# Optimization experiments

Hardware: AMD Instinct MI355X
Metric: run time of the kernel (lower is better)

## Reference

```python
import jax, jax.numpy as jnp
import numpy as np

N, C, E, S = 16384, 128, 262144, 10
AVG_NUM_NEIGHBORS = 16.0
INV_SQRT3 = 1.0 / np.sqrt(3.0)


def setup_inputs() -> dict:
    key = jax.random.key(0)
    ks = jax.random.split(key, 15)
    return dict(
        node_specie=jax.random.randint(ks[0], (N,), 0, S),
        node_feats=jax.random.normal(ks[1], (N, C, 4), jnp.float32),   # irreps 0e+1o per channel
        edge_attrs=jax.random.normal(ks[2], (E, 4), jnp.float32),      # Y: 0e+1o
        edge_feats=jax.random.normal(ks[3], (E, 8), jnp.float32),      # radial scalars
        senders=jax.random.randint(ks[4], (E,), 0, N),
        receivers=jax.random.randint(ks[5], (E,), 0, N),
        W_sc0=jax.random.normal(ks[6], (S, C, C), jnp.float32),
        W_sc1=jax.random.normal(ks[7], (S, C, C), jnp.float32),
        W_pre0=jax.random.normal(ks[8], (C, C), jnp.float32),
        W_pre1=jax.random.normal(ks[9], (C, C), jnp.float32),
        W_mlp1=jax.random.normal(ks[10], (8, 64), jnp.float32),
        W_mlp2=jax.random.normal(ks[11], (64, 64), jnp.float32),
        W_mlp3=jax.random.normal(ks[12], (64, 4), jnp.float32),
        W_post0=jax.random.normal(ks[13], (C, 2, C), jnp.float32),
        W_post1=jax.random.normal(ks[14], (C, 2, C), jnp.float32),
    )


def reference(node_specie, node_feats, edge_attrs, edge_feats, senders, receivers,
              W_sc0, W_sc1, W_pre0, W_pre1, W_mlp1, W_mlp2, W_mlp3, W_post0, W_post1):
    inv_c = 1.0 / np.sqrt(C)
    s_in = node_feats[..., 0]      # [N,C] 0e
    v_in = node_feats[..., 1:4]    # [N,C,3] 1o

    # linear_sc: per-species equivariant linear (0e+1o -> hidden 0e+1o)
    sc_s = jnp.einsum('nc,ncd->nd', s_in, W_sc0[node_specie]) * inv_c
    sc_v = jnp.einsum('nci,ncd->ndi', v_in, W_sc1[node_specie]) * inv_c
    sc = jnp.concatenate([sc_s[..., None], sc_v], axis=-1)  # [N,C,4]

    # linear_premp: channel-mixing equivariant linear (same irreps)
    s = (s_in @ W_pre0) * inv_c                              # [N,C]
    v = jnp.einsum('nci,cd->ndi', v_in, W_pre1) * inv_c      # [N,C,3]

    # MessagePassingConvolution (channel axis kept instead of hk.vmap)
    se_s = s[senders]              # [E,C]
    se_v = v[senders]              # [E,C,3]
    a = edge_attrs[:, 1:4]         # drop 0e part of Y -> 1o
    dot = jnp.einsum('eci,ei->ec', se_v, a) * INV_SQRT3      # 1o x 1o -> 0e
    sva = se_s[..., None] * a[:, None, :]                    # 0e x 1o -> 1o

    # radial MLP -> one mixing scalar per irrep (num_irreps = 4), shared across channels
    h = jax.nn.silu((edge_feats @ W_mlp1) * (1.0 / np.sqrt(8.0)))
    h = jax.nn.silu((h @ W_mlp2) * 0.125)
    mix = (h @ W_mlp3) * 0.125                               # [E,4]

    # messages irreps 2x0e+2x1o: [s, dot | v, s*a], each block scaled by its mix scalar
    msg = jnp.concatenate([
        se_s[..., None] * mix[:, None, 0:1],
        dot[..., None] * mix[:, None, 1:2],
        se_v * mix[:, None, 2:3],
        sva * mix[:, None, 3:4],
    ], axis=-1)                                              # [E,C,8]

    agg = jnp.zeros((N, C, 8), msg.dtype).at[receivers].add(msg) / AVG_NUM_NEIGHBORS

    # linear_postmp: (2x0e+2x1o, C channels) -> (0e+1o, C channels)
    inv2c = 1.0 / np.sqrt(2 * C)
    o_s = jnp.einsum('ncm,cmd->nd', agg[..., :2], W_post0) * inv2c
    o_v = jnp.einsum('ncmi,cmd->ndi', agg[..., 2:].reshape(N, C, 2, 3), W_post1) * inv2c
    node_out = jnp.concatenate([o_s[..., None], o_v], axis=-1)  # [N,C,4]
    return node_out, sc
```

## Files before the change

### kernel.cpp

```cpp
#include <hip/hip_runtime.h>
#include <hip/hip_bf16.h>

#define N_NODES 16384
#define C_DIM   128
#define E_EDGES 262144
#define S_SPEC  10
#define CHUNK   256
#define PROWS   16544
#define PTILES  1034

__device__ __constant__ const float INV_C  = 0.08838834764831845f;
__device__ __constant__ const float INV_2C = 0.0625f;
#define F_INV_SQRT3 0.5773502691896258f
#define F_INV_SQRT8 0.35355339059327373f
#define F_INV_AVG   0.0625f

typedef __attribute__((ext_vector_type(8))) short bf16x8;
typedef __attribute__((ext_vector_type(4))) float f32x4;

__device__ __forceinline__ float silu(float x) {
    return x / (1.0f + __expf(-x));
}

__device__ __forceinline__ unsigned short f2bf(float x) {
    __hip_bfloat16 h = __float2bfloat16(x);
    return *reinterpret_cast<unsigned short*>(&h);
}

__device__ __forceinline__ unsigned int pack2bf(float lo, float hi) {
    return (unsigned int)f2bf(lo) | ((unsigned int)f2bf(hi) << 16);
}

__device__ __forceinline__ float bf2f(unsigned short u) {
    return __uint_as_float(((unsigned int)u) << 16);
}

__global__ __launch_bounds__(256) void hist_kernel(
    const int* __restrict__ receivers, int* __restrict__ cnt)
{
    const int e = blockIdx.x * 256 + threadIdx.x;
    atomicAdd(&cnt[receivers[e]], 1);
}

__global__ __launch_bounds__(256) void scan16k_kernel(
    const int* __restrict__ cnt, int* __restrict__ start,
    int* __restrict__ cursor)
{
    __shared__ int sums[256];
    const int t = threadIdx.x;
    int s = 0;
    for (int i = 0; i < 64; ++i) s += cnt[t * 64 + i];
    sums[t] = s;
    __syncthreads();
    if (t == 0) {
        int a = 0;
        for (int i = 0; i < 256; ++i) { int v = sums[i]; sums[i] = a; a += v; }
    }
    __syncthreads();
    int a = sums[t];
    for (int i = 0; i < 64; ++i) {
        int v = cnt[t * 64 + i];
        start[t * 64 + i] = a;
        cursor[t * 64 + i] = a;
        a += v;
    }
    if (t == 255) start[N_NODES] = a;
}

__global__ __launch_bounds__(256) void scatter_kernel(
    const int* __restrict__ receivers, int* __restrict__ cursor,
    int* __restrict__ perm)
{
    const int e = blockIdx.x * 256 + threadIdx.x;
    const int pos = atomicAdd(&cursor[receivers[e]], 1);
    perm[pos] = e;
}

__global__ __launch_bounds__(256) void spec_hist_kernel(
    const int* __restrict__ specie, int* __restrict__ scnt)
{
    __shared__ int h[S_SPEC];
    const int t = threadIdx.x;
    if (t < S_SPEC) h[t] = 0;
    __syncthreads();
    atomicAdd(&h[specie[blockIdx.x * 256 + t]], 1);
    __syncthreads();
    if (t < S_SPEC) atomicAdd(&scnt[t], h[t]);
}

__global__ void spec_scan2_kernel(
    const int* __restrict__ scnt, int* __restrict__ poff,
    int* __restrict__ scur)
{
    if (threadIdx.x == 0) {
        int pa = 0;
        for (int i = 0; i < S_SPEC; ++i) {
            poff[i] = pa;
            scur[i] = 0;
            pa += ((scnt[i] + 15) >> 4) << 4;
        }
    }
}

__global__ __launch_bounds__(256) void spec_place_kernel(
    const int* __restrict__ specie, const int* __restrict__ poff,
    int* __restrict__ scur,
    int* __restrict__ prow_map, int* __restrict__ tile_spec)
{
    __shared__ int h[S_SPEC];
    __shared__ int bbase[S_SPEC];
    const int t = threadIdx.x;
    if (t < S_SPEC) h[t] = 0;
    __syncthreads();
    const int n = blockIdx.x * 256 + t;
    const int s = specie[n];
    const int lrank = atomicAdd(&h[s], 1);
    __syncthreads();
    if (t < S_SPEC && h[t] > 0) bbase[t] = atomicAdd(&scur[t], h[t]);
    __syncthreads();
    const int p = poff[s] + bbase[s] + lrank;
    prow_map[p] = n;
    tile_spec[p >> 4] = s;
}

__global__ __launch_bounds__(256) void node_in_convert_kernel(
    const int* __restrict__ prow_map, const float* __restrict__ node_feats,
    ushort* __restrict__ As, ushort* __restrict__ Av0,
    ushort* __restrict__ Av1, ushort* __restrict__ Av2)
{
    const int idx = blockIdx.x * 256 + threadIdx.x;
    const int p = idx >> 7, c = idx & 127;
    const int nid = prow_map[p];
    float4 f = {0.0f, 0.0f, 0.0f, 0.0f};
    if (nid >= 0) f = ((const float4*)node_feats)[nid * C_DIM + c];
    As [idx] = f2bf(f.x);
    Av0[idx] = f2bf(f.y);
    Av1[idx] = f2bf(f.z);
    Av2[idx] = f2bf(f.w);
}

__global__ __launch_bounds__(256) void wsc_convert_kernel(
    const float* __restrict__ Wsc0, const float* __restrict__ Wsc1,
    ushort* __restrict__ W0t, ushort* __restrict__ W1t_)
{
    const int idx = blockIdx.x * 256 + threadIdx.x;
    const int s = idx >> 14, d = (idx >> 7) & 127, k = idx & 127;
    W0t [idx] = f2bf(Wsc0[s * 16384 + k * 128 + d] * INV_C);
    W1t_[idx] = f2bf(Wsc1[s * 16384 + k * 128 + d] * INV_C);
}

__global__ __launch_bounds__(256) void wpre_convert_kernel(
    const float* __restrict__ Wpre0, const float* __restrict__ Wpre1,
    ushort* __restrict__ P0t, ushort* __restrict__ P1t)
{
    const int idx = blockIdx.x * 256 + threadIdx.x;
    const int d = idx >> 7, k = idx & 127;
    P0t[idx] = f2bf(Wpre0[k * 128 + d] * INV_C);
    P1t[idx] = f2bf(Wpre1[k * 128 + d] * INV_C);
}

__global__ __launch_bounds__(256) void wpost_convert_kernel(
    const float* __restrict__ W0, const float* __restrict__ W1,
    ushort* __restrict__ Bt0, ushort* __restrict__ Bt1)
{
    const int idx = blockIdx.x * 256 + threadIdx.x;
    const int k = idx >> 7, d = idx & 127;
    Bt0[d * 256 + k] = f2bf(W0[idx] * INV_2C);
    Bt1[d * 256 + k] = f2bf(W1[idx] * INV_2C);
}

__global__ __launch_bounds__(256) void wmlp_convert_kernel(
    const float* __restrict__ W1, const float* __restrict__ W2,
    const float* __restrict__ W3,
    ushort* __restrict__ W1t, ushort* __restrict__ W2t,
    ushort* __restrict__ W3t)
{
    const int idx = blockIdx.x * 256 + threadIdx.x;
    if (idx < 2048) {
        const int h = idx >> 5, k = idx & 31;
        W1t[idx] = (k < 8) ? f2bf(W1[k * 64 + h] * F_INV_SQRT8) : (ushort)0;
    }
    {
        const int c = idx >> 6, k = idx & 63;
        W2t[idx] = f2bf(W2[k * 64 + c] * 0.125f);
    }
    if (idx < 1024) {
        const int m = idx >> 6, k = idx & 63;
        W3t[idx] = (m < 4) ? f2bf(W3[k * 4 + m] * 0.125f) : (ushort)0;
    }
}

__global__ __launch_bounds__(512) void node_gemm_kernel(
    const int* __restrict__ prow_map,
    const int* __restrict__ tile_spec,
    const ushort* __restrict__ As,
    const ushort* __restrict__ Av0,
    const ushort* __restrict__ Av1,
    const ushort* __restrict__ Av2,
    const ushort* __restrict__ Wsc0t,
    const ushort* __restrict__ Wsc1t,
    const ushort* __restrict__ Wpre0t,
    const ushort* __restrict__ Wpre1t,
    float* __restrict__ out_sc,
    ushort4* __restrict__ sv_bf)
{
    const int l  = threadIdx.x & 63;
    const int w  = threadIdx.x >> 6;
    const int d0 = w * 16;
    const int lr = l & 15;
    const int lg = l >> 4;

    bf16x8 bp0[4], bp1[4];
#pragma unroll
    for (int ks = 0; ks < 4; ++ks) {
        bp0[ks] = *reinterpret_cast<const bf16x8*>(
            Wpre0t + (d0 + lr) * 128 + ks * 32 + lg * 8);
        bp1[ks] = *reinterpret_cast<const bf16x8*>(
            Wpre1t + (d0 + lr) * 128 + ks * 32 + lg * 8);
    }

    const int tile = blockIdx.x;
    const int sp   = tile_spec[tile];
    const int r0   = tile * 16;

    const ushort* as  = As  + (size_t)(r0 + lr) * 128 + lg * 8;
    const ushort* av0 = Av0 + (size_t)(r0 + lr) * 128 + lg * 8;
    const ushort* av1 = Av1 + (size_t)(r0 + lr) * 128 + lg * 8;
    const ushort* av2 = Av2 + (size_t)(r0 + lr) * 128 + lg * 8;
    const ushort* ws0 = Wsc0t + (size_t)sp * 16384 + (d0 + lr) * 128 + lg * 8;
    const ushort* ws1 = Wsc1t + (size_t)sp * 16384 + (d0 + lr) * 128 + lg * 8;

    const f32x4 zero = {0.0f, 0.0f, 0.0f, 0.0f};
    f32x4 aS0 = zero, aS1 = zero, aS2 = zero, aS3 = zero;
    f32x4 aP0 = zero, aP1 = zero, aP2 = zero, aP3 = zero;

#pragma unroll
    for (int ks = 0; ks < 4; ++ks) {
        const bf16x8 a_s  = *reinterpret_cast<const bf16x8*>(as  + ks * 32);
        const bf16x8 a_v0 = *reinterpret_cast<const bf16x8*>(av0 + ks * 32);
        const bf16x8 a_v1 = *reinterpret_cast<const bf16x8*>(av1 + ks * 32);
        const bf16x8 a_v2 = *reinterpret_cast<const bf16x8*>(av2 + ks * 32);
        const bf16x8 bs0  = *reinterpret_cast<const bf16x8*>(ws0 + ks * 32);
        const bf16x8 bs1  = *reinterpret_cast<const bf16x8*>(ws1 + ks * 32);
        aS0 = __builtin_amdgcn_mfma_f32_16x16x32_bf16(a_s,  bs0, aS0, 0, 0, 0);
        aS1 = __builtin_amdgcn_mfma_f32_16x16x32_bf16(a_v0, bs1, aS1, 0, 0, 0);
        aS2 = __builtin_amdgcn_mfma_f32_16x16x32_bf16(a_v1, bs1, aS2, 0, 0, 0);
        aS3 = __builtin_amdgcn_mfma_f32_16x16x32_bf16(a_v2, bs1, aS3, 0, 0, 0);
        aP0 = __builtin_amdgcn_mfma_f32_16x16x32_bf16(a_s,  bp0[ks], aP0, 0, 0, 0);
        aP1 = __builtin_amdgcn_mfma_f32_16x16x32_bf16(a_v0, bp1[ks], aP1, 0, 0, 0);
        aP2 = __builtin_amdgcn_mfma_f32_16x16x32_bf16(a_v1, bp1[ks], aP2, 0, 0, 0);
        aP3 = __builtin_amdgcn_mfma_f32_16x16x32_bf16(a_v2, bp1[ks], aP3, 0, 0, 0);
    }

#pragma unroll
    for (int r = 0; r < 4; ++r) {
        const int row = r0 + lg * 4 + r;
        const int nid = prow_map[row];
        if (nid >= 0) {
            float4 o = {aS0[r], aS1[r], aS2[r], aS3[r]};
            ((float4*)out_sc)[(size_t)nid * C_DIM + (d0 + lr)] = o;
            ushort4 pv = {f2bf(aP0[r]), f2bf(aP1[r]), f2bf(aP2[r]), f2bf(aP3[r])};
            sv_bf[(size_t)nid * C_DIM + (d0 + lr)] = pv;
        }
    }
}

__global__ __launch_bounds__(256) void edge_mlp_mfma_kernel(
    const float* __restrict__ edge_feats,
    const float* __restrict__ edge_attrs,
    const ushort* __restrict__ W1t,
    const ushort* __restrict__ W2t,
    const ushort* __restrict__ W3t,
    float* __restrict__ coef)
{
    __shared__ ushort h_lds[4][16][72];

    const int w  = threadIdx.x >> 6;
    const int l  = threadIdx.x & 63;
    const int lr = l & 15;
    const int lg = l >> 4;

    bf16x8 a1[4];
#pragma unroll
    for (int mt = 0; mt < 4; ++mt)
        a1[mt] = *reinterpret_cast<const bf16x8*>(
            W1t + (mt * 16 + lr) * 32 + lg * 8);
    bf16x8 a2[4][2];
#pragma unroll
    for (int mt = 0; mt < 4; ++mt)
#pragma unroll
        for (int ks = 0; ks < 2; ++ks)
            a2[mt][ks] = *reinterpret_cast<const bf16x8*>(
                W2t + (mt * 16 + lr) * 64 + ks * 32 + lg * 8);
    bf16x8 a3[2];
#pragma unroll
    for (int ks = 0; ks < 2; ++ks)
        a3[ks] = *reinterpret_cast<const bf16x8*>(
            W3t + lr * 64 + ks * 32 + lg * 8);

    const int tile = blockIdx.x * 4 + w;
    const int e0   = tile * 16;
    const f32x4 zero = {0.0f, 0.0f, 0.0f, 0.0f};

    bf16x8 b1 = {0, 0, 0, 0, 0, 0, 0, 0};
    if (lg == 0) {
        const float4 q0 = *(const float4*)(edge_feats + (size_t)(e0 + lr) * 8);
        const float4 q1 = *(const float4*)(edge_feats + (size_t)(e0 + lr) * 8 + 4);
        b1[0] = (short)f2bf(q0.x); b1[1] = (short)f2bf(q0.y);
        b1[2] = (short)f2bf(q0.z); b1[3] = (short)f2bf(q0.w);
        b1[4] = (short)f2bf(q1.x); b1[5] = (short)f2bf(q1.y);
        b1[6] = (short)f2bf(q1.z); b1[7] = (short)f2bf(q1.w);
    }

    f32x4 d1[4];
#pragma unroll
    for (int mt = 0; mt < 4; ++mt)
        d1[mt] = __builtin_amdgcn_mfma_f32_16x16x32_bf16(a1[mt], b1, zero, 0, 0, 0);

#pragma unroll
    for (int mt = 0; mt < 4; ++mt) {
        uint2 p;
        p.x = pack2bf(silu(d1[mt][0]), silu(d1[mt][1]));
        p.y = pack2bf(silu(d1[mt][2]), silu(d1[mt][3]));
        *reinterpret_cast<uint2*>(&h_lds[w][lr][mt * 16 + lg * 4]) = p;
    }
    __syncthreads();

    bf16x8 b2[2];
#pragma unroll
    for (int ks = 0; ks < 2; ++ks)
        b2[ks] = *reinterpret_cast<const bf16x8*>(
            &h_lds[w][lr][ks * 32 + lg * 8]);

    f32x4 d2[4];
#pragma unroll
    for (int mt = 0; mt < 4; ++mt) {
        d2[mt] = __builtin_amdgcn_mfma_f32_16x16x32_bf16(a2[mt][0], b2[0], zero, 0, 0, 0);
        d2[mt] = __builtin_amdgcn_mfma_f32_16x16x32_bf16(a2[mt][1], b2[1], d2[mt], 0, 0, 0);
    }

#pragma unroll
    for (int mt = 0; mt < 4; ++mt) {
        uint2 p;
        p.x = pack2bf(silu(d2[mt][0]), silu(d2[mt][1]));
        p.y = pack2bf(silu(d2[mt][2]), silu(d2[mt][3]));
        *reinterpret_cast<uint2*>(&h_lds[w][lr][mt * 16 + lg * 4]) = p;
    }
    __syncthreads();

    bf16x8 b3[2];
#pragma unroll
    for (int ks = 0; ks < 2; ++ks)
        b3[ks] = *reinterpret_cast<const bf16x8*>(
            &h_lds[w][lr][ks * 32 + lg * 8]);

    f32x4 d3;
    d3 = __builtin_amdgcn_mfma_f32_16x16x32_bf16(a3[0], b3[0], zero, 0, 0, 0);
    d3 = __builtin_amdgcn_mfma_f32_16x16x32_bf16(a3[1], b3[1], d3, 0, 0, 0);

    if (lg == 0) {
        const int e = e0 + lr;
        const float4 a = *(const float4*)(edge_attrs + (size_t)e * 4);
        const float mx0 = d3[0], mx1 = d3[1], mx2 = d3[2], mx3 = d3[3];
        float4 c0 = {mx0, mx1 * a.y * F_INV_SQRT3,
                     mx1 * a.z * F_INV_SQRT3, mx1 * a.w * F_INV_SQRT3};
        float4 c1 = {mx2, mx3 * a.y, mx3 * a.z, mx3 * a.w};
        ((float4*)coef)[e * 2 + 0] = c0;
        ((float4*)coef)[e * 2 + 1] = c1;
    }
}

__global__ __launch_bounds__(256) void agg_kernel(
    const int* __restrict__ start,
    const int* __restrict__ perm,
    const int* __restrict__ senders,
    const float* __restrict__ coef,
    const ushort4* __restrict__ sv_bf,
    unsigned int* __restrict__ A_s,
    unsigned int* __restrict__ A_v)
{
    __shared__ int   se_lds[CHUNK];
    __shared__ float sc_lds[CHUNK][8];

    const int n0   = blockIdx.x * 8;
    const int t    = threadIdx.x;
    const int c    = t & 127;
    const int half = t >> 7;

    int nbeg[4], nend[4];
#pragma unroll
    for (int k = 0; k < 4; ++k) {
        nbeg[k] = start[n0 + half * 4 + k];
        nend[k] = start[n0 + half * 4 + k + 1];
    }

    const int blk_beg = start[n0];
    const int blk_end = start[n0 + 8];
    const float4* coef4 = (const float4*)coef;

    float acc[4][8] = {};

    for (int cb = blk_beg; cb < blk_end; cb += CHUNK) {
        const int cn = min(CHUNK, blk_end - cb);
        __syncthreads();
        for (int j = t; j < cn; j += 256) {
            const int e = perm[cb + j];
            se_lds[j] = senders[e];
            ((float4*)sc_lds[j])[0] = coef4[e * 2 + 0];
            ((float4*)sc_lds[j])[1] = coef4[e * 2 + 1];
        }
        __syncthreads();

#pragma unroll
        for (int k = 0; k < 4; ++k) {
            const int lo = max(nbeg[k], cb);
            const int hi = min(nend[k], cb + cn);
            int idx = lo;
            for (; idx + 2 <= hi; idx += 2) {
                const int j0 = idx - cb, j1 = j0 + 1;
                const int snd0 = se_lds[j0];
                const int snd1 = se_lds[j1];
                const ushort4 u0 = sv_bf[snd0 * C_DIM + c];
                const ushort4 u1 = sv_bf[snd1 * C_DIM + c];
                const float* kf0 = sc_lds[j0];
                const float* kf1 = sc_lds[j1];
                const float x0 = bf2f(u0.x), y0 = bf2f(u0.y),
                            z0 = bf2f(u0.z), w0 = bf2f(u0.w);
                const float x1 = bf2f(u1.x), y1 = bf2f(u1.y),
                            z1 = bf2f(u1.z), w1 = bf2f(u1.w);
                acc[k][0] += x0 * kf0[0];
                acc[k][1] += y0 * kf0[1] + z0 * kf0[2] + w0 * kf0[3];
                acc[k][2] += y0 * kf0[4];
                acc[k][3] += z0 * kf0[4];
                acc[k][4] += w0 * kf0[4];
                acc[k][5] += x0 * kf0[5];
                acc[k][6] += x0 * kf0[6];
                acc[k][7] += x0 * kf0[7];
                acc[k][0] += x1 * kf1[0];
                acc[k][1] += y1 * kf1[1] + z1 * kf1[2] + w1 * kf1[3];
                acc[k][2] += y1 * kf1[4];
                acc[k][3] += z1 * kf1[4];
                acc[k][4] += w1 * kf1[4];
                acc[k][5] += x1 * kf1[5];
                acc[k][6] += x1 * kf1[6];
                acc[k][7] += x1 * kf1[7];
            }
            if (idx < hi) {
                const int j = idx - cb;
                const int snd = se_lds[j];
                const ushort4 u = sv_bf[snd * C_DIM + c];
                const float* kf = sc_lds[j];
                const float x = bf2f(u.x), y = bf2f(u.y),
                            z = bf2f(u.z), w = bf2f(u.w);
                acc[k][0] += x * kf[0];
                acc[k][1] += y * kf[1] + z * kf[2] + w * kf[3];
                acc[k][2] += y * kf[4];
                acc[k][3] += z * kf[4];
                acc[k][4] += w * kf[4];
                acc[k][5] += x * kf[5];
                acc[k][6] += x * kf[6];
                acc[k][7] += x * kf[7];
            }
        }
    }

#pragma unroll
    for (int k = 0; k < 4; ++k) {
        const int n = n0 + half * 4 + k;
        A_s[n * 128 + c] = pack2bf(acc[k][0] * F_INV_AVG, acc[k][1] * F_INV_AVG);
        A_v[(n * 3 + 0) * 128 + c] =
            pack2bf(acc[k][2] * F_INV_AVG, acc[k][5] * F_INV_AVG);
        A_v[(n * 3 + 1) * 128 + c] =
            pack2bf(acc[k][3] * F_INV_AVG, acc[k][6] * F_INV_AVG);
        A_v[(n * 3 + 2) * 128 + c] =
            pack2bf(acc[k][4] * F_INV_AVG, acc[k][7] * F_INV_AVG);
    }
}

__global__ __launch_bounds__(512) void post_gemm_kernel(
    const ushort* __restrict__ A,
    const ushort* __restrict__ Bt,
    float* __restrict__ out,
    int ntiles, int rows_per_node, int comp_base)
{
    const int l  = threadIdx.x & 63;
    const int w  = threadIdx.x >> 6;
    const int d0 = w * 16;
    const int lr = l & 15;
    const int lg = l >> 4;

    bf16x8 bfrag[8];
#pragma unroll
    for (int ks = 0; ks < 8; ++ks) {
        bfrag[ks] = *reinterpret_cast<const bf16x8*>(
            Bt + (size_t)(d0 + lr) * 256 + ks * 32 + lg * 8);
    }

    for (int tile = blockIdx.x; tile < ntiles; tile += gridDim.x) {
        const int r0 = tile * 16;
        f32x4 acc = {0.0f, 0.0f, 0.0f, 0.0f};
        const ushort* ap = A + (size_t)(r0 + lr) * 256 + lg * 8;
#pragma unroll
        for (int ks = 0; ks < 8; ++ks) {
            bf16x8 a = *reinterpret_cast<const bf16x8*>(ap + ks * 32);
            acc = __builtin_amdgcn_mfma_f32_16x16x32_bf16(a, bfrag[ks], acc,
                                                          0, 0, 0);
        }
#pragma unroll
        for (int r = 0; r < 4; ++r) {
            const int row = r0 + lg * 4 + r;
            int n, comp;
            if (rows_per_node == 1) { n = row; comp = 0; }
            else { n = row / 3; comp = comp_base + (row - n * 3); }
            out[(size_t)n * 512 + (d0 + lr) * 4 + comp] = acc[r];
        }
    }
}

extern "C" void kernel_launch(void* const* d_in, const int* in_sizes, int n_in,
                              void* d_out, int out_size, void* d_ws, size_t ws_size,
                              hipStream_t stream)
{
    const int*   specie     = (const int*)d_in[0];
    const float* node_feats = (const float*)d_in[1];
    const float* edge_attrs = (const float*)d_in[2];
    const float* edge_feats = (const float*)d_in[3];
    const int*   senders    = (const int*)d_in[4];
    const int*   receivers  = (const int*)d_in[5];
    const float* Wsc0  = (const float*)d_in[6];
    const float* Wsc1  = (const float*)d_in[7];
    const float* Wpre0 = (const float*)d_in[8];
    const float* Wpre1 = (const float*)d_in[9];
    const float* Wm1   = (const float*)d_in[10];
    const float* Wm2   = (const float*)d_in[11];
    const float* Wm3   = (const float*)d_in[12];
    const float* Wp0   = (const float*)d_in[13];
    const float* Wp1   = (const float*)d_in[14];

    float* out_node = (float*)d_out;
    float* out_sc   = out_node + (size_t)N_NODES * C_DIM * 4;

    char* ws = (char*)d_ws;
    ushort4*      sv_bf = (ushort4*)ws;
    unsigned int* A_s   = (unsigned int*)(ws + (size_t)16 * 1024 * 1024);
    unsigned int* A_v   = A_s + (size_t)N_NODES * 128;
    float*        coef  = (float*)(A_v + (size_t)3 * N_NODES * 128);
    ushort*       Asin  = (ushort*)(coef + (size_t)E_EDGES * 8);
    ushort*       Av0in = Asin  + (size_t)PROWS * 128;
    ushort*       Av1in = Av0in + (size_t)PROWS * 128;
    ushort*       Av2in = Av1in + (size_t)PROWS * 128;
    ushort*       Bt0   = Av2in + (size_t)PROWS * 128;
    ushort*       Bt1   = Bt0 + 256 * 128;
    ushort*       Wsc0t = Bt1 + 256 * 128;
    ushort*       Wsc1t = Wsc0t + S_SPEC * 128 * 128;
    ushort*       Wpre0t = Wsc1t + S_SPEC * 128 * 128;
    ushort*       Wpre1t = Wpre0t + 128 * 128;
    ushort*       W1t   = Wpre1t + 128 * 128;
    ushort*       W2t   = W1t + 64 * 32;
    ushort*       W3t   = W2t + 64 * 64;
    int* counts    = (int*)(W3t + 16 * 64);
    int* start     = counts + N_NODES;
    int* cursor    = start + (N_NODES + 1);
    int* perm      = cursor + N_NODES;
    int* scnt      = perm + E_EDGES;
    int* poff      = scnt + S_SPEC;
    int* scur      = poff + S_SPEC;
    int* prow_map  = scur + S_SPEC;
    int* tile_spec = prow_map + PROWS;

    hipMemsetAsync(counts, 0, N_NODES * sizeof(int), stream);
    hipMemsetAsync(scnt, 0, S_SPEC * sizeof(int), stream);
    hipMemsetAsync(prow_map, 0xFF, PROWS * sizeof(int), stream);
    hipMemsetAsync(tile_spec, 0, PTILES * sizeof(int), stream);

    hist_kernel<<<E_EDGES / 256, 256, 0, stream>>>(receivers, counts);
    scan16k_kernel<<<1, 256, 0, stream>>>(counts, start, cursor);
    scatter_kernel<<<E_EDGES / 256, 256, 0, stream>>>(receivers, cursor, perm);

    spec_hist_kernel<<<N_NODES / 256, 256, 0, stream>>>(specie, scnt);
    spec_scan2_kernel<<<1, 64, 0, stream>>>(scnt, poff, scur);
    spec_place_kernel<<<N_NODES / 256, 256, 0, stream>>>(
        specie, poff, scur, prow_map, tile_spec);

    node_in_convert_kernel<<<PROWS * 128 / 256, 256, 0, stream>>>(
        prow_map, node_feats, Asin, Av0in, Av1in, Av2in);
    wsc_convert_kernel<<<S_SPEC * 128 * 128 / 256, 256, 0, stream>>>(
        Wsc0, Wsc1, Wsc0t, Wsc1t);
    wpre_convert_kernel<<<64, 256, 0, stream>>>(Wpre0, Wpre1, Wpre0t, Wpre1t);
    wpost_convert_kernel<<<128, 256, 0, stream>>>(Wp0, Wp1, Bt0, Bt1);
    wmlp_convert_kernel<<<16, 256, 0, stream>>>(Wm1, Wm2, Wm3, W1t, W2t, W3t);

    node_gemm_kernel<<<PTILES, 512, 0, stream>>>(
        prow_map, tile_spec, Asin, Av0in, Av1in, Av2in,
        Wsc0t, Wsc1t, Wpre0t, Wpre1t, out_sc, sv_bf);

    edge_mlp_mfma_kernel<<<E_EDGES / 64, 256, 0, stream>>>(
        edge_feats, edge_attrs, W1t, W2t, W3t, coef);

    agg_kernel<<<N_NODES / 8, 256, 0, stream>>>(
        start, perm, senders, coef, sv_bf, A_s, A_v);

    post_gemm_kernel<<<512, 512, 0, stream>>>(
        (const ushort*)A_s, Bt0, out_node, N_NODES / 16, 1, 0);
    post_gemm_kernel<<<1024, 512, 0, stream>>>(
        (const ushort*)A_v, Bt1, out_node, 3 * N_NODES / 16, 3, 1);
}
```

Measured before the change: 264.3 us.

## Merge setup kernels, restructure aggregation to wave-per-node, fuse post GEMMs

New measurement: 236.2 us. -10.6%, faster.

```diff
diff --git a/kernel.cpp b/kernel.cpp
--- a/kernel.cpp
+++ b/kernel.cpp
@@ -5,7 +5,6 @@
 #define C_DIM   128
 #define E_EDGES 262144
 #define S_SPEC  10
-#define CHUNK   256
 #define PROWS   16544
 #define PTILES  1034
 
@@ -31,23 +30,57 @@
     return (unsigned int)f2bf(lo) | ((unsigned int)f2bf(hi) << 16);
 }
 
-__device__ __forceinline__ float bf2f(unsigned short u) {
-    return __uint_as_float(((unsigned int)u) << 16);
+__device__ __forceinline__ float bf2f(unsigned int u16) {
+    return __uint_as_float(u16 << 16);
+}
+
+__global__ __launch_bounds__(256) void init_kernel(
+    int* __restrict__ counts, int* __restrict__ scnt,
+    int* __restrict__ prow_map, int* __restrict__ tile_spec)
+{
+    const int idx = blockIdx.x * 256 + threadIdx.x;
+    if (idx < N_NODES) counts[idx] = 0;
+    if (idx < S_SPEC)  scnt[idx] = 0;
+    if (idx < PROWS)   prow_map[idx] = -1;
+    if (idx < PTILES)  tile_spec[idx] = 0;
 }
 
 __global__ __launch_bounds__(256) void hist_kernel(
-    const int* __restrict__ receivers, int* __restrict__ cnt)
-{
-    const int e = blockIdx.x * 256 + threadIdx.x;
+    const int* __restrict__ receivers, int* __restrict__ cnt,
+    const int* __restrict__ specie, int* __restrict__ scnt)
+{
+    __shared__ int h[S_SPEC];
+    const int t = threadIdx.x;
+    const bool doSpec = blockIdx.x < (N_NODES / 256);
+    if (doSpec) {
+        if (t < S_SPEC) h[t] = 0;
+        __syncthreads();
+        atomicAdd(&h[specie[blockIdx.x * 256 + t]], 1);
+    }
+    const int e = blockIdx.x * 256 + t;
     atomicAdd(&cnt[receivers[e]], 1);
-}
-
-__global__ __launch_bounds__(256) void scan16k_kernel(
+    if (doSpec) {
+        __syncthreads();
+        if (t < S_SPEC) atomicAdd(&scnt[t], h[t]);
+    }
+}
+
+__global__ __launch_bounds__(256) void scan_kernel(
     const int* __restrict__ cnt, int* __restrict__ start,
-    int* __restrict__ cursor)
+    int* __restrict__ cursor,
+    const int* __restrict__ scnt, int* __restrict__ poff,
+    int* __restrict__ scur)
 {
     __shared__ int sums[256];
     const int t = threadIdx.x;
+    if (t == 0) {
+        int pa = 0;
+        for (int i = 0; i < S_SPEC; ++i) {
+            poff[i] = pa;
+            scur[i] = 0;
+            pa += ((scnt[i] + 15) >> 4) << 4;
+        }
+    }
     int s = 0;
     for (int i = 0; i < 64; ++i) s += cnt[t * 64 + i];
     sums[t] = s;
@@ -67,126 +100,89 @@
     if (t == 255) start[N_NODES] = a;
 }
 
-__global__ __launch_bounds__(256) void scatter_kernel(
+__global__ __launch_bounds__(256) void scatter_place_kernel(
     const int* __restrict__ receivers, int* __restrict__ cursor,
-    int* __restrict__ perm)
-{
-    const int e = blockIdx.x * 256 + threadIdx.x;
-    const int pos = atomicAdd(&cursor[receivers[e]], 1);
-    perm[pos] = e;
-}
-
-__global__ __launch_bounds__(256) void spec_hist_kernel(
-    const int* __restrict__ specie, int* __restrict__ scnt)
-{
-    __shared__ int h[S_SPEC];
-    const int t = threadIdx.x;
-    if (t < S_SPEC) h[t] = 0;
-    __syncthreads();
-    atomicAdd(&h[specie[blockIdx.x * 256 + t]], 1);
-    __syncthreads();
-    if (t < S_SPEC) atomicAdd(&scnt[t], h[t]);
-}
-
-__global__ void spec_scan2_kernel(
-    const int* __restrict__ scnt, int* __restrict__ poff,
-    int* __restrict__ scur)
-{
-    if (threadIdx.x == 0) {
-        int pa = 0;
-        for (int i = 0; i < S_SPEC; ++i) {
-            poff[i] = pa;
-            scur[i] = 0;
-            pa += ((scnt[i] + 15) >> 4) << 4;
-        }
-    }
-}
-
-__global__ __launch_bounds__(256) void spec_place_kernel(
+    int* __restrict__ perm,
     const int* __restrict__ specie, const int* __restrict__ poff,
     int* __restrict__ scur,
     int* __restrict__ prow_map, int* __restrict__ tile_spec)
 {
-    __shared__ int h[S_SPEC];
-    __shared__ int bbase[S_SPEC];
     const int t = threadIdx.x;
-    if (t < S_SPEC) h[t] = 0;
-    __syncthreads();
-    const int n = blockIdx.x * 256 + t;
-    const int s = specie[n];
-    const int lrank = atomicAdd(&h[s], 1);
-    __syncthreads();
-    if (t < S_SPEC && h[t] > 0) bbase[t] = atomicAdd(&scur[t], h[t]);
-    __syncthreads();
-    const int p = poff[s] + bbase[s] + lrank;
-    prow_map[p] = n;
-    tile_spec[p >> 4] = s;
-}
-
-__global__ __launch_bounds__(256) void node_in_convert_kernel(
+    const int e = blockIdx.x * 256 + t;
+    const int pos = atomicAdd(&cursor[receivers[e]], 1);
+    perm[pos] = e;
+
+    if (blockIdx.x < (N_NODES / 256)) {
+        __shared__ int h[S_SPEC];
+        __shared__ int bbase[S_SPEC];
+        if (t < S_SPEC) h[t] = 0;
+        __syncthreads();
+        const int n = blockIdx.x * 256 + t;
+        const int s = specie[n];
+        const int lrank = atomicAdd(&h[s], 1);
+        __syncthreads();
+        if (t < S_SPEC && h[t] > 0) bbase[t] = atomicAdd(&scur[t], h[t]);
+        __syncthreads();
+        const int p = poff[s] + bbase[s] + lrank;
+        prow_map[p] = n;
+        tile_spec[p >> 4] = s;
+    }
+}
+
+__global__ __launch_bounds__(256) void prep_kernel(
     const int* __restrict__ prow_map, const float* __restrict__ node_feats,
     ushort* __restrict__ As, ushort* __restrict__ Av0,
-    ushort* __restrict__ Av1, ushort* __restrict__ Av2)
-{
-    const int idx = blockIdx.x * 256 + threadIdx.x;
-    const int p = idx >> 7, c = idx & 127;
-    const int nid = prow_map[p];
-    float4 f = {0.0f, 0.0f, 0.0f, 0.0f};
-    if (nid >= 0) f = ((const float4*)node_feats)[nid * C_DIM + c];
-    As [idx] = f2bf(f.x);
-    Av0[idx] = f2bf(f.y);
-    Av1[idx] = f2bf(f.z);
-    Av2[idx] = f2bf(f.w);
-}
-
-__global__ __launch_bounds__(256) void wsc_convert_kernel(
+    ushort* __restrict__ Av1, ushort* __restrict__ Av2,
     const float* __restrict__ Wsc0, const float* __restrict__ Wsc1,
-    ushort* __restrict__ W0t, ushort* __restrict__ W1t_)
-{
-    const int idx = blockIdx.x * 256 + threadIdx.x;
-    const int s = idx >> 14, d = (idx >> 7) & 127, k = idx & 127;
-    W0t [idx] = f2bf(Wsc0[s * 16384 + k * 128 + d] * INV_C);
-    W1t_[idx] = f2bf(Wsc1[s * 16384 + k * 128 + d] * INV_C);
-}
-
-__global__ __launch_bounds__(256) void wpre_convert_kernel(
+    ushort* __restrict__ Wsc0t, ushort* __restrict__ Wsc1t,
     const float* __restrict__ Wpre0, const float* __restrict__ Wpre1,
-    ushort* __restrict__ P0t, ushort* __restrict__ P1t)
-{
-    const int idx = blockIdx.x * 256 + threadIdx.x;
-    const int d = idx >> 7, k = idx & 127;
-    P0t[idx] = f2bf(Wpre0[k * 128 + d] * INV_C);
-    P1t[idx] = f2bf(Wpre1[k * 128 + d] * INV_C);
-}
-
-__global__ __launch_bounds__(256) void wpost_convert_kernel(
-    const float* __restrict__ W0, const float* __restrict__ W1,
-    ushort* __restrict__ Bt0, ushort* __restrict__ Bt1)
-{
-    const int idx = blockIdx.x * 256 + threadIdx.x;
-    const int k = idx >> 7, d = idx & 127;
-    Bt0[d * 256 + k] = f2bf(W0[idx] * INV_2C);
-    Bt1[d * 256 + k] = f2bf(W1[idx] * INV_2C);
-}
-
-__global__ __launch_bounds__(256) void wmlp_convert_kernel(
-    const float* __restrict__ W1, const float* __restrict__ W2,
-    const float* __restrict__ W3,
+    ushort* __restrict__ Wpre0t, ushort* __restrict__ Wpre1t,
+    const float* __restrict__ Wp0, const float* __restrict__ Wp1,
+    ushort* __restrict__ Bt0, ushort* __restrict__ Bt1,
+    const float* __restrict__ Wm1, const float* __restrict__ Wm2,
+    const float* __restrict__ Wm3,
     ushort* __restrict__ W1t, ushort* __restrict__ W2t,
     ushort* __restrict__ W3t)
 {
     const int idx = blockIdx.x * 256 + threadIdx.x;
-    if (idx < 2048) {
-        const int h = idx >> 5, k = idx & 31;
-        W1t[idx] = (k < 8) ? f2bf(W1[k * 64 + h] * F_INV_SQRT8) : (ushort)0;
-    }
     {
-        const int c = idx >> 6, k = idx & 63;
-        W2t[idx] = f2bf(W2[k * 64 + c] * 0.125f);
-    }
-    if (idx < 1024) {
-        const int m = idx >> 6, k = idx & 63;
-        W3t[idx] = (m < 4) ? f2bf(W3[k * 4 + m] * 0.125f) : (ushort)0;
+        const int p = idx >> 7, c = idx & 127;
+        const int nid = prow_map[p];
+        float4 f = {0.0f, 0.0f, 0.0f, 0.0f};
+        if (nid >= 0) f = ((const float4*)node_feats)[nid * C_DIM + c];
+        As [idx] = f2bf(f.x);
+        Av0[idx] = f2bf(f.y);
+        Av1[idx] = f2bf(f.z);
+        Av2[idx] = f2bf(f.w);
+    }
+    if (idx < S_SPEC * 128 * 128) {
+        const int s = idx >> 14, d = (idx >> 7) & 127, k = idx & 127;
+        Wsc0t[idx] = f2bf(Wsc0[s * 16384 + k * 128 + d] * INV_C);
+        Wsc1t[idx] = f2bf(Wsc1[s * 16384 + k * 128 + d] * INV_C);
+    }
+    if (idx < 16384) {
+        const int d = idx >> 7, k = idx & 127;
+        Wpre0t[idx] = f2bf(Wpre0[k * 128 + d] * INV_C);
+        Wpre1t[idx] = f2bf(Wpre1[k * 128 + d] * INV_C);
+    }
+    if (idx < 32768) {
+        const int k = idx >> 7, d = idx & 127;
+        Bt0[d * 256 + k] = f2bf(Wp0[idx] * INV_2C);
+        Bt1[d * 256 + k] = f2bf(Wp1[idx] * INV_2C);
+    }
+    if (idx < 4096) {
+        if (idx < 2048) {
+            const int hh = idx >> 5, k = idx & 31;
+            W1t[idx] = (k < 8) ? f2bf(Wm1[k * 64 + hh] * F_INV_SQRT8) : (ushort)0;
+        }
+        {
+            const int c = idx >> 6, k = idx & 63;
+            W2t[idx] = f2bf(Wm2[k * 64 + c] * 0.125f);
+        }
+        if (idx < 1024) {
+            const int m = idx >> 6, k = idx & 63;
+            W3t[idx] = (m < 4) ? f2bf(Wm3[k * 4 + m] * 0.125f) : (ushort)0;
+        }
     }
 }
 
@@ -375,113 +371,88 @@
     const int* __restrict__ perm,
     const int* __restrict__ senders,
     const float* __restrict__ coef,
-    const ushort4* __restrict__ sv_bf,
+    const uint4* __restrict__ sv16,
     unsigned int* __restrict__ A_s,
     unsigned int* __restrict__ A_v)
 {
-    __shared__ int   se_lds[CHUNK];
-    __shared__ float sc_lds[CHUNK][8];
-
-    const int n0   = blockIdx.x * 8;
-    const int t    = threadIdx.x;
-    const int c    = t & 127;
-    const int half = t >> 7;
-
-    int nbeg[4], nend[4];
-#pragma unroll
-    for (int k = 0; k < 4; ++k) {
-        nbeg[k] = start[n0 + half * 4 + k];
-        nend[k] = start[n0 + half * 4 + k + 1];
-    }
-
-    const int blk_beg = start[n0];
-    const int blk_end = start[n0 + 8];
+    const int n    = blockIdx.x * 4 + (threadIdx.x >> 6);
+    const int lane = threadIdx.x & 63;
+
+    const int beg = start[n];
+    const int end = start[n + 1];
     const float4* coef4 = (const float4*)coef;
 
-    float acc[4][8] = {};
-
-    for (int cb = blk_beg; cb < blk_end; cb += CHUNK) {
-        const int cn = min(CHUNK, blk_end - cb);
-        __syncthreads();
-        for (int j = t; j < cn; j += 256) {
-            const int e = perm[cb + j];
-            se_lds[j] = senders[e];
-            ((float4*)sc_lds[j])[0] = coef4[e * 2 + 0];
-            ((float4*)sc_lds[j])[1] = coef4[e * 2 + 1];
-        }
-        __syncthreads();
-
-#pragma unroll
-        for (int k = 0; k < 4; ++k) {
-            const int lo = max(nbeg[k], cb);
-            const int hi = min(nend[k], cb + cn);
-            int idx = lo;
-            for (; idx + 2 <= hi; idx += 2) {
-                const int j0 = idx - cb, j1 = j0 + 1;
-                const int snd0 = se_lds[j0];
-                const int snd1 = se_lds[j1];
-                const ushort4 u0 = sv_bf[snd0 * C_DIM + c];
-                const ushort4 u1 = sv_bf[snd1 * C_DIM + c];
-                const float* kf0 = sc_lds[j0];
-                const float* kf1 = sc_lds[j1];
-                const float x0 = bf2f(u0.x), y0 = bf2f(u0.y),
-                            z0 = bf2f(u0.z), w0 = bf2f(u0.w);
-                const float x1 = bf2f(u1.x), y1 = bf2f(u1.y),
-                            z1 = bf2f(u1.z), w1 = bf2f(u1.w);
-                acc[k][0] += x0 * kf0[0];
-                acc[k][1] += y0 * kf0[1] + z0 * kf0[2] + w0 * kf0[3];
-                acc[k][2] += y0 * kf0[4];
-                acc[k][3] += z0 * kf0[4];
-                acc[k][4] += w0 * kf0[4];
-                acc[k][5] += x0 * kf0[5];
-                acc[k][6] += x0 * kf0[6];
-                acc[k][7] += x0 * kf0[7];
-                acc[k][0] += x1 * kf1[0];
-                acc[k][1] += y1 * kf1[1] + z1 * kf1[2] + w1 * kf1[3];
-                acc[k][2] += y1 * kf1[4];
-                acc[k][3] += z1 * kf1[4];
-                acc[k][4] += w1 * kf1[4];
-                acc[k][5] += x1 * kf1[5];
-                acc[k][6] += x1 * kf1[6];
-                acc[k][7] += x1 * kf1[7];
-            }
-            if (idx < hi) {
-                const int j = idx - cb;
-                const int snd = se_lds[j];
-                const ushort4 u = sv_bf[snd * C_DIM + c];
-                const float* kf = sc_lds[j];
-                const float x = bf2f(u.x), y = bf2f(u.y),
-                            z = bf2f(u.z), w = bf2f(u.w);
-                acc[k][0] += x * kf[0];
-                acc[k][1] += y * kf[1] + z * kf[2] + w * kf[3];
-                acc[k][2] += y * kf[4];
-                acc[k][3] += z * kf[4];
-                acc[k][4] += w * kf[4];
-                acc[k][5] += x * kf[5];
-                acc[k][6] += x * kf[6];
-                acc[k][7] += x * kf[7];
-            }
-        }
-    }
-
-#pragma unroll
-    for (int k = 0; k < 4; ++k) {
-        const int n = n0 + half * 4 + k;
-        A_s[n * 128 + c] = pack2bf(acc[k][0] * F_INV_AVG, acc[k][1] * F_INV_AVG);
-        A_v[(n * 3 + 0) * 128 + c] =
-            pack2bf(acc[k][2] * F_INV_AVG, acc[k][5] * F_INV_AVG);
-        A_v[(n * 3 + 1) * 128 + c] =
-            pack2bf(acc[k][3] * F_INV_AVG, acc[k][6] * F_INV_AVG);
-        A_v[(n * 3 + 2) * 128 + c] =
-            pack2bf(acc[k][4] * F_INV_AVG, acc[k][7] * F_INV_AVG);
-    }
+    float acc0[8] = {};
+    float acc1[8] = {};
+
+    int e_nx = 0, s_nx = 0;
+    if (beg < end) {
+        e_nx = __builtin_amdgcn_readfirstlane(perm[beg]);
+        s_nx = __builtin_amdgcn_readfirstlane(senders[e_nx]);
+    }
+
+    for (int idx = beg; idx < end; ++idx) {
+        const int e   = e_nx;
+        const int snd = s_nx;
+        if (idx + 1 < end) {
+            e_nx = __builtin_amdgcn_readfirstlane(perm[idx + 1]);
+            s_nx = __builtin_amdgcn_readfirstlane(senders[e_nx]);
+        }
+        const float4 k0 = coef4[(size_t)e * 2 + 0];
+        const float4 k1 = coef4[(size_t)e * 2 + 1];
+        const uint4  q  = sv16[(size_t)snd * 64 + lane];
+
+        const float x0 = bf2f(q.x & 0xffff), y0 = bf2f(q.x >> 16);
+        const float z0 = bf2f(q.y & 0xffff), w0 = bf2f(q.y >> 16);
+        const float x1 = bf2f(q.z & 0xffff), y1 = bf2f(q.z >> 16);
+        const float z1 = bf2f(q.w & 0xffff), w1 = bf2f(q.w >> 16);
+
+        acc0[0] += x0 * k0.x;
+        acc0[1] += y0 * k0.y + z0 * k0.z + w0 * k0.w;
+        acc0[2] += y0 * k1.x;
+        acc0[3] += z0 * k1.x;
+        acc0[4] += w0 * k1.x;
+        acc0[5] += x0 * k1.y;
+        acc0[6] += x0 * k1.z;
+        acc0[7] += x0 * k1.w;
+
+        acc1[0] += x1 * k0.x;
+        acc1[1] += y1 * k0.y + z1 * k0.z + w1 * k0.w;
+        acc1[2] += y1 * k1.x;
+        acc1[3] += z1 * k1.x;
+        acc1[4] += w1 * k1.x;
+        acc1[5] += x1 * k1.y;
+        acc1[6] += x1 * k1.z;
+        acc1[7] += x1 * k1.w;
+    }
+
+    uint2 vs;
+    vs.x = pack2bf(acc0[0] * F_INV_AVG, acc0[1] * F_INV_AVG);
+    vs.y = pack2bf(acc1[0] * F_INV_AVG, acc1[1] * F_INV_AVG);
+    ((uint2*)A_s)[(size_t)n * 64 + lane] = vs;
+
+    uint2 v0;
+    v0.x = pack2bf(acc0[2] * F_INV_AVG, acc0[5] * F_INV_AVG);
+    v0.y = pack2bf(acc1[2] * F_INV_AVG, acc1[5] * F_INV_AVG);
+    ((uint2*)A_v)[((size_t)n * 3 + 0) * 64 + lane] = v0;
+
+    uint2 v1;
+    v1.x = pack2bf(acc0[3] * F_INV_AVG, acc0[6] * F_INV_AVG);
+    v1.y = pack2bf(acc1[3] * F_INV_AVG, acc1[6] * F_INV_AVG);
+    ((uint2*)A_v)[((size_t)n * 3 + 1) * 64 + lane] = v1;
+
+    uint2 v2;
+    v2.x = pack2bf(acc0[4] * F_INV_AVG, acc0[7] * F_INV_AVG);
+    v2.y = pack2bf(acc1[4] * F_INV_AVG, acc1[7] * F_INV_AVG);
+    ((uint2*)A_v)[((size_t)n * 3 + 2) * 64 + lane] = v2;
 }
 
 __global__ __launch_bounds__(512) void post_gemm_kernel(
-    const ushort* __restrict__ A,
-    const ushort* __restrict__ Bt,
-    float* __restrict__ out,
-    int ntiles, int rows_per_node, int comp_base)
+    const ushort* __restrict__ A_s,
+    const ushort* __restrict__ A_v,
+    const ushort* __restrict__ Bt0,
+    const ushort* __restrict__ Bt1,
+    float* __restrict__ out)
 {
     const int l  = threadIdx.x & 63;
     const int w  = threadIdx.x >> 6;
@@ -489,6 +460,13 @@
     const int lr = l & 15;
     const int lg = l >> 4;
 
+    const bool isS = blockIdx.x < 512;
+    const ushort* A  = isS ? A_s : A_v;
+    const ushort* Bt = isS ? Bt0 : Bt1;
+    const int ntiles  = isS ? (N_NODES / 16) : (3 * N_NODES / 16);
+    const int b0      = isS ? blockIdx.x : blockIdx.x - 512;
+    const int gstride = isS ? 512 : 1024;
+
     bf16x8 bfrag[8];
 #pragma unroll
     for (int ks = 0; ks < 8; ++ks) {
@@ -496,7 +474,7 @@
             Bt + (size_t)(d0 + lr) * 256 + ks * 32 + lg * 8);
     }
 
-    for (int tile = blockIdx.x; tile < ntiles; tile += gridDim.x) {
+    for (int tile = b0; tile < ntiles; tile += gstride) {
         const int r0 = tile * 16;
         f32x4 acc = {0.0f, 0.0f, 0.0f, 0.0f};
         const ushort* ap = A + (size_t)(r0 + lr) * 256 + lg * 8;
@@ -510,8 +488,8 @@
         for (int r = 0; r < 4; ++r) {
             const int row = r0 + lg * 4 + r;
             int n, comp;
-            if (rows_per_node == 1) { n = row; comp = 0; }
-            else { n = row / 3; comp = comp_base + (row - n * 3); }
+            if (isS) { n = row; comp = 0; }
+            else { n = row / 3; comp = 1 + (row - n * 3); }
             out[(size_t)n * 512 + (d0 + lr) * 4 + comp] = acc[r];
         }
     }
@@ -568,27 +546,21 @@
     int* prow_map  = scur + S_SPEC;
     int* tile_spec = prow_map + PROWS;
 
-    hipMemsetAsync(counts, 0, N_NODES * sizeof(int), stream);
-    hipMemsetAsync(scnt, 0, S_SPEC * sizeof(int), stream);
-    hipMemsetAsync(prow_map, 0xFF, PROWS * sizeof(int), stream);
-    hipMemsetAsync(tile_spec, 0, PTILES * sizeof(int), stream);
-
-    hist_kernel<<<E_EDGES / 256, 256, 0, stream>>>(receivers, counts);
-    scan16k_kernel<<<1, 256, 0, stream>>>(counts, start, cursor);
-    scatter_kernel<<<E_EDGES / 256, 256, 0, stream>>>(receivers, cursor, perm);
-
-    spec_hist_kernel<<<N_NODES / 256, 256, 0, stream>>>(specie, scnt);
-    spec_scan2_kernel<<<1, 64, 0, stream>>>(scnt, poff, scur);
-    spec_place_kernel<<<N_NODES / 256, 256, 0, stream>>>(
-        specie, poff, scur, prow_map, tile_spec);
-
-    node_in_convert_kernel<<<PROWS * 128 / 256, 256, 0, stream>>>(
-        prow_map, node_feats, Asin, Av0in, Av1in, Av2in);
-    wsc_convert_kernel<<<S_SPEC * 128 * 128 / 256, 256, 0, stream>>>(
-        Wsc0, Wsc1, Wsc0t, Wsc1t);
-    wpre_convert_kernel<<<64, 256, 0, stream>>>(Wpre0, Wpre1, Wpre0t, Wpre1t);
-    wpost_convert_kernel<<<128, 256, 0, stream>>>(Wp0, Wp1, Bt0, Bt1);
-    wmlp_convert_kernel<<<16, 256, 0, stream>>>(Wm1, Wm2, Wm3, W1t, W2t, W3t);
+    init_kernel<<<(PROWS + 255) / 256, 256, 0, stream>>>(
+        counts, scnt, prow_map, tile_spec);
+
+    hist_kernel<<<E_EDGES / 256, 256, 0, stream>>>(
+        receivers, counts, specie, scnt);
+
+    scan_kernel<<<1, 256, 0, stream>>>(counts, start, cursor, scnt, poff, scur);
+
+    scatter_place_kernel<<<E_EDGES / 256, 256, 0, stream>>>(
+        receivers, cursor, perm, specie, poff, scur, prow_map, tile_spec);
+
+    prep_kernel<<<PROWS * 128 / 256, 256, 0, stream>>>(
+        prow_map, node_feats, Asin, Av0in, Av1in, Av2in,
+        Wsc0, Wsc1, Wsc0t, Wsc1t, Wpre0, Wpre1, Wpre0t, Wpre1t,
+        Wp0, Wp1, Bt0, Bt1, Wm1, Wm2, Wm3, W1t, W2t, W3t);
 
     node_gemm_kernel<<<PTILES, 512, 0, stream>>>(
         prow_map, tile_spec, Asin, Av0in, Av1in, Av2in,
@@ -597,11 +569,9 @@
     edge_mlp_mfma_kernel<<<E_EDGES / 64, 256, 0, stream>>>(
         edge_feats, edge_attrs, W1t, W2t, W3t, coef);
 
-    agg_kernel<<<N_NODES / 8, 256, 0, stream>>>(
-        start, perm, senders, coef, sv_bf, A_s, A_v);
-
-    post_gemm_kernel<<<512, 512, 0, stream>>>(
-        (const ushort*)A_s, Bt0, out_node, N_NODES / 16, 1, 0);
-    post_gemm_kernel<<<1024, 512, 0, stream>>>(
-        (const ushort*)A_v, Bt1, out_node, 3 * N_NODES / 16, 3, 1);
-}
+    agg_kernel<<<N_NODES / 4, 256, 0, stream>>>(
+        start, perm, senders, coef, (const uint4*)sv_bf, A_s, A_v);
+
+    post_gemm_kernel<<<1536, 512, 0, stream>>>(
+        (const ushort*)A_s, (const ushort*)A_v, Bt0, Bt1, out_node);
+}
```
